# Kernel tuning notes

Hardware: AMD Instinct MI355X
Metric: run time of the kernel (lower is better)

## Reference

```python
import jax, jax.numpy as jnp
import numpy as np

B, S, D, H, NH = 128, 512, 64, 256, 8
HD = H // NH
NEG = -10000000000.0


def _ln(x, g, b, eps=1e-5):
    m = x.mean(-1, keepdims=True)
    v = ((x - m) ** 2).mean(-1, keepdims=True)
    return (x - m) * jax.lax.rsqrt(v + eps) * g + b


def _mha(xq, xkv, mask, qW, qb, kW, kb, vW, vb, oW, ob):
    # mask: [B,1,1,S_kv] bool, True = masked out
    b, sq, _ = xq.shape
    sk = xkv.shape[1]
    Q = (xq @ qW + qb).reshape(b, sq, NH, HD).transpose(0, 2, 1, 3)
    K = (xkv @ kW + kb).reshape(b, sk, NH, HD).transpose(0, 2, 1, 3)
    V = (xkv @ vW + vb).reshape(b, sk, NH, HD).transpose(0, 2, 1, 3)
    energy = jnp.einsum('bhqd,bhkd->bhqk', Q, K) / jnp.sqrt(jnp.float32(HD))
    energy = jnp.where(mask, NEG, energy)
    attn = jax.nn.softmax(energy, axis=-1)  # dropout is identity in eval
    x = jnp.einsum('bhqk,bhkd->bhqd', attn, V)
    x = x.transpose(0, 2, 1, 3).reshape(b, sq, H)
    return x @ oW + ob


def _ffn(x, f1W, f1b, f2W, f2b):
    # NewGELU == tanh-approximate GELU (GPT-2)
    return jax.nn.gelu(x @ f1W + f1b, approximate=True) @ f2W + f2b


def _fwd(src, ln0sg, ln0sb, ln0tg, ln0tb, semW, semb, temW, temb,
         e_qW, e_qb, e_kW, e_kb, e_vW, e_vb, e_oW, e_ob, e_ln1g, e_ln1b,
         e_f1W, e_f1b, e_f2W, e_f2b, e_ln2g, e_ln2b,
         d_sqW, d_sqb, d_skW, d_skb, d_svW, d_svb, d_soW, d_sob, d_ln1g, d_ln1b,
         d_eqW, d_eqb, d_ekW, d_ekb, d_evW, d_evb, d_eoW, d_eob, d_ln2g, d_ln2b,
         d_f1W, d_f1b, d_f2W, d_f2b, d_ln3g, d_ln3b, outW, outb):
    valid = src.sum(-1) != 0                      # [B,S] (prod_fea == 0)
    amask = (~valid)[:, None, None, :]            # [B,1,1,S]; trg==src so trg_mask==src_mask
    embs_src = _ln(src, ln0sg, ln0sb) @ semW + semb   # emb_need
    embs_trg = _ln(src, ln0tg, ln0tb) @ temW + temb
    # encoder layer
    a = _mha(embs_src, embs_src, amask, e_qW, e_qb, e_kW, e_kb, e_vW, e_vb, e_oW, e_ob)
    x = _ln(embs_src + a, e_ln1g, e_ln1b)
    enc_src = _ln(x + _ffn(x, e_f1W, e_f1b, e_f2W, e_f2b), e_ln2g, e_ln2b)
    # decoder layer
    a = _mha(embs_trg, embs_trg, amask, d_sqW, d_sqb, d_skW, d_skb, d_svW, d_svb, d_soW, d_sob)
    t = _ln(embs_trg + a, d_ln1g, d_ln1b)
    a = _mha(t, enc_src, amask, d_eqW, d_eqb, d_ekW, d_ekb, d_evW, d_evb, d_eoW, d_eob)
    t = _ln(t + a, d_ln2g, d_ln2b)
    t = _ln(t + _ffn(t, d_f1W, d_f1b, d_f2W, d_f2b), d_ln3g, d_ln3b)
    logits = (t @ outW + outb)[..., 0]            # [B,S]
    p = jnp.exp(logits) * valid.astype(logits.dtype)
    return p / p.sum(-1, keepdims=True)           # multi_purchase=False branch


def setup_inputs() -> dict:
    key = jax.random.key(0)
    keys = iter(jax.random.split(key, 64))
    inp = {"src": jax.random.normal(next(keys), (B, S, D), dtype=jnp.float32)}

    def lin(name, i, o):
        inp[name + "W"] = jax.random.normal(next(keys), (i, o), dtype=jnp.float32) * 0.02
        inp[name + "b"] = jnp.zeros((o,), dtype=jnp.float32)

    def ln(name, d):
        inp[name + "g"] = jnp.ones((d,), dtype=jnp.float32)
        inp[name + "b"] = jnp.zeros((d,), dtype=jnp.float32)

    ln("ln0s", D); ln("ln0t", D)
    lin("sem", D, H); lin("tem", D, H)
    for n in ["e_q", "e_k", "e_v", "e_o"]:
        lin(n, H, H)
    ln("e_ln1", H); lin("e_f1", H, H); lin("e_f2", H, H); ln("e_ln2", H)
    for n in ["d_sq", "d_sk", "d_sv", "d_so", "d_eq", "d_ek", "d_ev", "d_eo"]:
        lin(n, H, H)
    ln("d_ln1", H); ln("d_ln2", H)
    lin("d_f1", H, H); lin("d_f2", H, H); ln("d_ln3", H)
    lin("out", H, 1)
    return inp


def reference(src, ln0sg, ln0sb, ln0tg, ln0tb, semW, semb, temW, temb,
              e_qW, e_qb, e_kW, e_kb, e_vW, e_vb, e_oW, e_ob, e_ln1g, e_ln1b,
              e_f1W, e_f1b, e_f2W, e_f2b, e_ln2g, e_ln2b,
              d_sqW, d_sqb, d_skW, d_skb, d_svW, d_svb, d_soW, d_sob, d_ln1g, d_ln1b,
              d_eqW, d_eqb, d_ekW, d_ekb, d_evW, d_evb, d_eoW, d_eob, d_ln2g, d_ln2b,
              d_f1W, d_f1b, d_f2W, d_f2b, d_ln3g, d_ln3b, outW, outb):
    return _fwd(src, ln0sg, ln0sb, ln0tg, ln0tb, semW, semb, temW, temb,
                e_qW, e_qb, e_kW, e_kb, e_vW, e_vb, e_oW, e_ob, e_ln1g, e_ln1b,
                e_f1W, e_f1b, e_f2W, e_f2b, e_ln2g, e_ln2b,
                d_sqW, d_sqb, d_skW, d_skb, d_svW, d_svb, d_soW, d_sob, d_ln1g, d_ln1b,
                d_eqW, d_eqb, d_ekW, d_ekb, d_evW, d_evb, d_eoW, d_eob, d_ln2g, d_ln2b,
                d_f1W, d_f1b, d_f2W, d_f2b, d_ln3g, d_ln3b, outW, outb)
```

## Files before the change

kernel.cpp:

```cpp
#include <hip/hip_runtime.h>
#include <hip/hip_bf16.h>


#define Bb  128
#define Ss  512
#define Hh  256
#define NHh 8
#define Mm  (Bb*Ss)

typedef unsigned short bf16_t;
typedef __attribute__((ext_vector_type(8))) short short8;
typedef __attribute__((ext_vector_type(4))) float f32x4;

__device__ __forceinline__ float bf2f(bf16_t h){
  union { unsigned int u; float f; } v; v.u = ((unsigned int)h)<<16; return v.f;
}
__device__ __forceinline__ bf16_t f2bf(float f){
  union { float f; unsigned int u; } v; v.f = f;
  unsigned int r = (v.u + 0x7fffu + ((v.u>>16)&1u)) >> 16;
  return (bf16_t)r;
}
__device__ __forceinline__ unsigned pk_bf16(float a, float b){
  union { __hip_bfloat162 h; unsigned u; } v;
  v.h = __float22bfloat162_rn(float2{a,b});
  return v.u;
}
__device__ __forceinline__ short8 ld_bf8(const bf16_t* p){
  union { uint4 u; short8 s; } v; v.u = *(const uint4*)p; return v.s;
}
__device__ __forceinline__ void gload16(const bf16_t* g, bf16_t* l){
  __builtin_amdgcn_global_load_lds(
      (const __attribute__((address_space(1))) void*)g,
      (__attribute__((address_space(3))) void*)l, 16, 0, 0);
}
__device__ __forceinline__ float exp2_hw(float x){
  float r; asm("v_exp_f32 %0, %1" : "=v"(r) : "v"(x)); return r;
}
__device__ __forceinline__ float gelu_f(float x){
  float u = 0.7978845608028654f*(x + 0.044715f*x*x*x);
  float e = __expf(2.0f*u);
  float th = 1.0f - 2.0f*__builtin_amdgcn_rcpf(e + 1.0f);
  return 0.5f*x*(1.0f + th);
}

struct PrepDesc { const float* s; unsigned off; int K; };
struct Prep18  { PrepDesc d[18]; };

__global__ __launch_bounds__(256) void k_prep(Prep18 p, bf16_t* __restrict__ arena)
{
  PrepDesc dd = p.d[blockIdx.y];
  int i = blockIdx.x*256 + threadIdx.x;
  if (i < dd.K*256){
    int k = i>>8, n = i&255;
    arena[dd.off + n*dd.K + k] = f2bf(dd.s[i]);
  }
}

__global__ __launch_bounds__(256) void k_ln0(const float* __restrict__ src,
    const float* __restrict__ gs, const float* __restrict__ bs,
    const float* __restrict__ gt, const float* __restrict__ bt,
    bf16_t* __restrict__ xs, bf16_t* __restrict__ xt, float* __restrict__ valid)
{
  int row  = blockIdx.x*4 + (threadIdx.x>>6);
  int lane = threadIdx.x & 63;
  float x = src[(size_t)row*64 + lane];
  float s = x;
  #pragma unroll
  for (int o=32;o>0;o>>=1) s += __shfl_xor(s,o);
  float mean = s*(1.0f/64.0f);
  float d = x - mean;
  float ss = d*d;
  #pragma unroll
  for (int o=32;o>0;o>>=1) ss += __shfl_xor(ss,o);
  float r = rsqrtf(ss*(1.0f/64.0f) + 1e-5f);
  float xn = d*r;
  xs[(size_t)row*64+lane] = f2bf(xn*gs[lane] + bs[lane]);
  xt[(size_t)row*64+lane] = f2bf(xn*gt[lane] + bt[lane]);
  if (lane==0) valid[row] = (s != 0.0f) ? 1.0f : 0.0f;
}

template<int EPI, int OUTM, int KK>
__global__ __launch_bounds__(512,2) void k_wgemm(const bf16_t* __restrict__ A,
    const bf16_t* __restrict__ Wt, const float* __restrict__ bias,
    void* __restrict__ Cv, const bf16_t* __restrict__ Pres,
    const float* __restrict__ g, const float* __restrict__ bb,
    const float* __restrict__ oW, const float* __restrict__ obp, float cs)
{
  constexpr int NKC  = KK/32;
  constexpr int IDS  = 16*NKC;
  constexpr int PERW = IDS/8;
  __shared__ bf16_t Ws[IDS*512];

  int t = threadIdx.x, w = t>>6, lane = t&63, l15 = lane&15, quad = lane>>4;
  int r0 = blockIdx.x*256 + w*32;

  #pragma unroll
  for (int j=0; j<PERW; j++){
    int id = w*PERW + j; int kc = id>>4, nt = id&15;
    gload16(Wt + (size_t)(nt*16 + l15)*KK + kc*32 + quad*8, &Ws[id*512]);
  }
  short8 a0 = ld_bf8(A + (size_t)(r0      + l15)*KK + quad*8);
  short8 a1 = ld_bf8(A + (size_t)(r0 + 16 + l15)*KK + quad*8);
  __syncthreads();

  f32x4 z = {0.f,0.f,0.f,0.f};
  f32x4 acc0[16], acc1[16];
  #pragma unroll
  for (int nt=0; nt<16; nt++){ acc0[nt] = z; acc1[nt] = z; }

  #pragma unroll
  for (int kc=0; kc<NKC; kc++){
    short8 a0n, a1n;
    if (kc+1 < NKC){
      a0n = ld_bf8(A + (size_t)(r0      + l15)*KK + (kc+1)*32 + quad*8);
      a1n = ld_bf8(A + (size_t)(r0 + 16 + l15)*KK + (kc+1)*32 + quad*8);
    }
    #pragma unroll
    for (int nt=0; nt<16; nt++){
      short8 b = ld_bf8(&Ws[(kc*16 + nt)*512 + lane*8]);
      acc0[nt] = __builtin_amdgcn_mfma_f32_16x16x32_bf16(a0, b, acc0[nt], 0,0,0);
      acc1[nt] = __builtin_amdgcn_mfma_f32_16x16x32_bf16(a1, b, acc1[nt], 0,0,0);
    }
    a0 = a0n; a1 = a1n;
  }

  float bv[16];
  #pragma unroll
  for (int nt=0; nt<16; nt++) bv[nt] = bias[nt*16 + l15];

  if (OUTM==0){
    auto epi = [&](f32x4 (&ac)[16], int tt){
      int rowb = r0 + tt*16 + quad*4;
      #pragma unroll
      for (int nt=0; nt<16; nt++)
        #pragma unroll
        for (int r=0; r<4; r++){
          float v = ac[nt][r] + bv[nt];
          v = (EPI==1) ? gelu_f(v) : v*cs;
          ((bf16_t*)Cv)[(size_t)(rowb + r)*256 + nt*16 + l15] = f2bf(v);
        }
    };
    epi(acc0, 0); epi(acc1, 1);
  } else if (OUTM==2){
    auto epi = [&](f32x4 (&ac)[16], int tt){
      int m = r0 + tt*16 + quad*4;
      #pragma unroll
      for (int nt=0; nt<16; nt++){
        int col = nt*16 + l15;
        uint2 pk = { pk_bf16(ac[nt][0]+bv[nt], ac[nt][1]+bv[nt]),
                     pk_bf16(ac[nt][2]+bv[nt], ac[nt][3]+bv[nt]) };
        *(uint2*)&((bf16_t*)Cv)[((size_t)((m>>9)*256 + col))*512 + (m&511)] = pk;
      }
    };
    epi(acc0, 0); epi(acc1, 1);
  } else {
    float gv[16], bbv[16], wv[16];
    #pragma unroll
    for (int nt=0; nt<16; nt++){ gv[nt] = g[nt*16+l15]; bbv[nt] = bb[nt*16+l15]; }
    if (OUTM==5)
      #pragma unroll
      for (int nt=0; nt<16; nt++) wv[nt] = oW[nt*16+l15];
    float ob0 = (OUTM==5) ? obp[0] : 0.f;

    auto epi = [&](f32x4 (&ac)[16], int tt){
      #pragma unroll
      for (int r=0; r<4; r++){
        int row = r0 + tt*16 + quad*4 + r;
        const bf16_t* pr = Pres + (size_t)row*256;
        float v[16]; float s = 0.f, q = 0.f;
        #pragma unroll
        for (int nt=0; nt<16; nt++){
          v[nt] = ac[nt][r] + bv[nt] + bf2f(pr[nt*16 + l15]);
          s += v[nt]; q += v[nt]*v[nt];
        }
        s += __shfl_xor(s,1); s += __shfl_xor(s,2);
        s += __shfl_xor(s,4); s += __shfl_xor(s,8);
        q += __shfl_xor(q,1); q += __shfl_xor(q,2);
        q += __shfl_xor(q,4); q += __shfl_xor(q,8);
        float mean = s*(1.0f/256.0f);
        float var  = q*(1.0f/256.0f) - mean*mean;
        float rstd = rsqrtf(var + 1e-5f);
        if (OUTM==3){
          bf16_t* po = (bf16_t*)Cv + (size_t)row*256;
          #pragma unroll
          for (int nt=0; nt<16; nt++)
            po[nt*16 + l15] = f2bf((v[nt]-mean)*rstd*gv[nt] + bbv[nt]);
        } else {
          float s2 = 0.f;
          #pragma unroll
          for (int nt=0; nt<16; nt++)
            s2 += ((v[nt]-mean)*rstd*gv[nt] + bbv[nt]) * wv[nt];
          s2 += __shfl_xor(s2,1); s2 += __shfl_xor(s2,2);
          s2 += __shfl_xor(s2,4); s2 += __shfl_xor(s2,8);
          if (l15==0) ((float*)Cv)[row] = s2 + ob0;
        }
      }
    };
    epi(acc0, 0); epi(acc1, 1);
  }
}

__global__ __launch_bounds__(256) void k_attn(const bf16_t* __restrict__ Qm,
    const bf16_t* __restrict__ Km, const bf16_t* __restrict__ VT,
    const float* __restrict__ valid, bf16_t* __restrict__ AO)
{
  __shared__ bf16_t Pbuf[4][2][2][16][40];
  __shared__ float  Smask[512];
  int t = threadIdx.x, wave = t>>6, lane = t&63, l15 = lane&15, quad = lane>>4;
  int lid = blockIdx.x + 8*blockIdx.y + 1024*blockIdx.z;
  int hp = lid & 3, pb = (lid>>2)&1, g = (lid>>3)&7, bh = lid>>6;
  int h  = hp*2 + (g&1);
  int qc = g>>1;
  int b  = bh*2 + pb;
  int q0 = qc*128;

  Smask[t]     = (valid[b*Ss + t      ] != 0.f) ? 0.f : -1.44269504e10f;
  Smask[t+256] = (valid[b*Ss + t + 256] != 0.f) ? 0.f : -1.44269504e10f;
  __syncthreads();

  short8 aQ0 = ld_bf8(Qm + (size_t)(b*Ss + q0 + (wave*2  )*16 + l15)*256 + h*32 + quad*8);
  short8 aQ1 = ld_bf8(Qm + (size_t)(b*Ss + q0 + (wave*2+1)*16 + l15)*256 + h*32 + quad*8);
  const bf16_t* Kb = Km + (size_t)(b*Ss)*256 + h*32;
  const bf16_t* Vb = VT + ((size_t)b*256 + h*32)*512;

  f32x4 z = {0.f,0.f,0.f,0.f};
  f32x4 O0[2] = {z,z}, O1[2] = {z,z};
  float ls0 = 0.f, ls1 = 0.f;

  auto process = [&](int kt2n, short8 K0, short8 K1){
    int s = kt2n & 1;
    #pragma unroll
    for (int half=0; half<2; half++){
      short8 aK = half ? K1 : K0;
      int ktile = kt2n*2 + half;
      __builtin_amdgcn_s_setprio(1);
      f32x4 s0 = __builtin_amdgcn_mfma_f32_16x16x32_bf16(aK, aQ0, z, 0,0,0);
      f32x4 s1 = __builtin_amdgcn_mfma_f32_16x16x32_bf16(aK, aQ1, z, 0,0,0);
      __builtin_amdgcn_s_setprio(0);
      float4 mb = *(const float4*)&Smask[ktile*16 + quad*4];
      float p00 = exp2_hw(s0[0] + mb.x);
      float p01 = exp2_hw(s0[1] + mb.y);
      float p02 = exp2_hw(s0[2] + mb.z);
      float p03 = exp2_hw(s0[3] + mb.w);
      float p10 = exp2_hw(s1[0] + mb.x);
      float p11 = exp2_hw(s1[1] + mb.y);
      float p12 = exp2_hw(s1[2] + mb.z);
      float p13 = exp2_hw(s1[3] + mb.w);
      ls0 += (p00+p01)+(p02+p03);
      ls1 += (p10+p11)+(p12+p13);
      uint2 w0 = { pk_bf16(p00,p01), pk_bf16(p02,p03) };
      uint2 w1 = { pk_bf16(p10,p11), pk_bf16(p12,p13) };
      *(uint2*)&Pbuf[wave][0][s][l15][half*16 + quad*4] = w0;
      *(uint2*)&Pbuf[wave][1][s][l15][half*16 + quad*4] = w1;
    }
  };
  auto loadK = [&](int n, short8& K0, short8& K1){
    K0 = ld_bf8(Kb + (size_t)((n*2  )*16 + l15)*256 + quad*8);
    K1 = ld_bf8(Kb + (size_t)((n*2+1)*16 + l15)*256 + quad*8);
  };
  auto loadV = [&](int n, short8& V0, short8& V1){
    V0 = ld_bf8(Vb + (size_t)(l15   )*512 + n*32 + quad*8);
    V1 = ld_bf8(Vb + (size_t)(16+l15)*512 + n*32 + quad*8);
  };

  short8 cK0, cK1, pK0, pK1, nK0, nK1;
  short8 cV0, cV1, mV0, mV1, nV0, nV1;
  loadK(0, cK0, cK1);
  process(0, cK0, cK1);
  loadK(1, pK0, pK1);
  loadV(0, cV0, cV1);
  loadV(1, mV0, mV1);

  #pragma unroll 2
  for (int kt2=0; kt2<16; kt2++){
    if (kt2+2 < 16){ loadK(kt2+2, nK0, nK1); loadV(kt2+2, nV0, nV1); }
    int s = kt2 & 1;
    short8 aP0 = ld_bf8(&Pbuf[wave][0][s][l15][quad*8]);
    short8 aP1 = ld_bf8(&Pbuf[wave][1][s][l15][quad*8]);
    __builtin_amdgcn_s_setprio(1);
    O0[0] = __builtin_amdgcn_mfma_f32_16x16x32_bf16(aP0, cV0, O0[0], 0,0,0);
    O0[1] = __builtin_amdgcn_mfma_f32_16x16x32_bf16(aP0, cV1, O0[1], 0,0,0);
    O1[0] = __builtin_amdgcn_mfma_f32_16x16x32_bf16(aP1, cV0, O1[0], 0,0,0);
    O1[1] = __builtin_amdgcn_mfma_f32_16x16x32_bf16(aP1, cV1, O1[1], 0,0,0);
    __builtin_amdgcn_s_setprio(0);
    if (kt2+1 < 16) process(kt2+1, pK0, pK1);
    pK0 = nK0; pK1 = nK1;
    cV0 = mV0; cV1 = mV1; mV0 = nV0; mV1 = nV1;
  }

  ls0 += __shfl_xor(ls0,16); ls0 += __shfl_xor(ls0,32);
  ls1 += __shfl_xor(ls1,16); ls1 += __shfl_xor(ls1,32);
  float linv0 = (ls0 > 0.f) ? 1.0f/ls0 : 0.f;
  float linv1 = (ls1 > 0.f) ? 1.0f/ls1 : 0.f;
  float i0[4], i1[4];
  #pragma unroll
  for (int r=0; r<4; r++){
    i0[r] = __shfl(linv0, quad*4 + r);
    i1[r] = __shfl(linv1, quad*4 + r);
  }
  size_t r0 = (size_t)(b*Ss + q0 + (wave*2  )*16);
  size_t r1 = (size_t)(b*Ss + q0 + (wave*2+1)*16);
  #pragma unroll
  for (int nt=0; nt<2; nt++)
    #pragma unroll
    for (int r=0; r<4; r++){
      AO[(r0 + quad*4 + r)*256 + h*32 + nt*16 + l15] = f2bf(O0[nt][r]*i0[r]);
      AO[(r1 + quad*4 + r)*256 + h*32 + nt*16 + l15] = f2bf(O1[nt][r]*i1[r]);
    }
}

__global__ __launch_bounds__(256) void k_final(const float* __restrict__ L,
    const float* __restrict__ valid, float* __restrict__ out)
{
  __shared__ float wsum[4];
  int b = blockIdx.x, t = threadIdx.x;
  float e0 = __expf(L[b*Ss + t      ]) * valid[b*Ss + t      ];
  float e1 = __expf(L[b*Ss + 256 + t]) * valid[b*Ss + 256 + t];
  float s = e0 + e1;
  #pragma unroll
  for (int o=32;o>0;o>>=1) s += __shfl_xor(s,o);
  if ((t&63)==0) wsum[t>>6] = s;
  __syncthreads();
  float tot = wsum[0]+wsum[1]+wsum[2]+wsum[3];
  out[b*Ss + t      ] = e0/tot;
  out[b*Ss + 256 + t] = e1/tot;
}

extern "C" void kernel_launch(void* const* d_in, const int* in_sizes, int n_in,
                              void* d_out, int out_size, void* d_ws, size_t ws_size,
                              hipStream_t stream)
{
  #define F(i) ((const float*)d_in[(i)])
  bool sig = (in_sizes[33] == 256);
  const float* d_eqW  = F(sig?35:33); const float* d_eqb  = F(sig?36:34);
  const float* d_ekW  = F(sig?37:35); const float* d_ekb  = F(sig?38:36);
  const float* d_evW  = F(sig?39:37); const float* d_evb  = F(sig?40:38);
  const float* d_eoW  = F(sig?41:39); const float* d_eob  = F(sig?42:40);
  const float* d_ln1g = F(sig?33:41); const float* d_ln1b = F(sig?34:42);

  char* w = (char*)d_ws;
  bf16_t* P0 = (bf16_t*)w; w += (size_t)Mm*Hh*2;
  bf16_t* P1 = (bf16_t*)w; w += (size_t)Mm*Hh*2;
  bf16_t* H0 = (bf16_t*)w; w += (size_t)Mm*Hh*2;
  bf16_t* H1 = (bf16_t*)w;
  bf16_t* xs = (bf16_t*)w; w += (size_t)Mm*Hh*2;
  bf16_t* H2 = (bf16_t*)w;
  bf16_t* xt = (bf16_t*)w; w += (size_t)Mm*Hh*2;
  bf16_t* Wa = (bf16_t*)w; w += (size_t)(2*16384 + 16*65536)*2;
  float*  valid  = (float*)w; w += (size_t)Mm*4;
  float*  logits = (float*)w; w += (size_t)Mm*4;
  float* out = (float*)d_out;

  unsigned o_sem = 0, o_tem = 16384;
  unsigned o_w[16]; for (int i=0;i<16;i++) o_w[i] = 32768 + i*65536u;
  Prep18 pp;
  const float* srcs[18] = { F(5), F(7), F(9), F(11), F(13), F(15), F(19), F(21),
                            F(25), F(27), F(29), F(31), d_eqW, d_ekW, d_evW, d_eoW,
                            F(45), F(47) };
  unsigned offs[18] = { o_sem, o_tem, o_w[0],o_w[1],o_w[2],o_w[3],o_w[4],o_w[5],
                        o_w[6],o_w[7],o_w[8],o_w[9],o_w[10],o_w[11],o_w[12],o_w[13],
                        o_w[14],o_w[15] };
  for (int i=0;i<18;i++){ pp.d[i].s = srcs[i]; pp.d[i].off = offs[i]; pp.d[i].K = (i<2)?64:256; }

  dim3 blk(256);
  dim3 blk512(512);
  dim3 gLN(Mm/4);
  dim3 gW(256);
  dim3 gA(NHh, Bb, 4);
  dim3 gP(256, 18);
  const float* NF = nullptr; const bf16_t* NB = nullptr;
  const float QS = 0.17677669529663687f * 1.4426950408889634f;

  k_prep<<<gP, blk, 0, stream>>>(pp, Wa);
  k_ln0<<<gLN, blk, 0, stream>>>(F(0), F(1),F(2), F(3),F(4), xs, xt, valid);

  k_wgemm<0,0,64><<<gW, blk512, 0, stream>>>(xs, Wa+o_sem, F(6), P0, NB, NF,NF,NF,NF, 1.0f);
  k_wgemm<0,0,64><<<gW, blk512, 0, stream>>>(xt, Wa+o_tem, F(8), P1, NB, NF,NF,NF,NF, 1.0f);

  k_wgemm<0,0,256><<<gW, blk512, 0, stream>>>(P0, Wa+o_w[0], F(10), H0, NB, NF,NF,NF,NF, QS);
  k_wgemm<0,0,256><<<gW, blk512, 0, stream>>>(P0, Wa+o_w[1], F(12), H1, NB, NF,NF,NF,NF, 1.0f);
  k_wgemm<0,2,256><<<gW, blk512, 0, stream>>>(P0, Wa+o_w[2], F(14), H2, NB, NF,NF,NF,NF, 1.0f);
  k_attn<<<gA, blk, 0, stream>>>(H0, H1, H2, valid, H0);
  k_wgemm<0,3,256><<<gW, blk512, 0, stream>>>(H0, Wa+o_w[3], F(16), P0, P0, F(17),F(18), NF,NF, 1.0f);
  k_wgemm<1,0,256><<<gW, blk512, 0, stream>>>(P0, Wa+o_w[4], F(20), H0, NB, NF,NF,NF,NF, 1.0f);
  k_wgemm<0,3,256><<<gW, blk512, 0, stream>>>(H0, Wa+o_w[5], F(22), P0, P0, F(23),F(24), NF,NF, 1.0f);

  k_wgemm<0,0,256><<<gW, blk512, 0, stream>>>(P1, Wa+o_w[6], F(26), H0, NB, NF,NF,NF,NF, QS);
  k_wgemm<0,0,256><<<gW, blk512, 0, stream>>>(P1, Wa+o_w[7], F(28), H1, NB, NF,NF,NF,NF, 1.0f);
  k_wgemm<0,2,256><<<gW, blk512, 0, stream>>>(P1, Wa+o_w[8], F(30), H2, NB, NF,NF,NF,NF, 1.0f);
  k_attn<<<gA, blk, 0, stream>>>(H0, H1, H2, valid, H0);
  k_wgemm<0,3,256><<<gW, blk512, 0, stream>>>(H0, Wa+o_w[9], F(32), P1, P1, d_ln1g,d_ln1b, NF,NF, 1.0f);

  k_wgemm<0,0,256><<<gW, blk512, 0, stream>>>(P1, Wa+o_w[10], d_eqb, H0, NB, NF,NF,NF,NF, QS);
  k_wgemm<0,0,256><<<gW, blk512, 0, stream>>>(P0, Wa+o_w[11], d_ekb, H1, NB, NF,NF,NF,NF, 1.0f);
  k_wgemm<0,2,256><<<gW, blk512, 0, stream>>>(P0, Wa+o_w[12], d_evb, H2, NB, NF,NF,NF,NF, 1.0f);
  k_attn<<<gA, blk, 0, stream>>>(H0, H1, H2, valid, H0);
  k_wgemm<0,3,256><<<gW, blk512, 0, stream>>>(H0, Wa+o_w[13], d_eob, P1, P1, F(43),F(44), NF,NF, 1.0f);

  k_wgemm<1,0,256><<<gW, blk512, 0, stream>>>(P1, Wa+o_w[14], F(46), H0, NB, NF,NF,NF,NF, 1.0f);
  k_wgemm<0,5,256><<<gW, blk512, 0, stream>>>(H0, Wa+o_w[15], F(48), logits, P1, F(49),F(50), F(51),F(52), 1.0f);

  k_final<<<dim3(Bb), blk, 0, stream>>>(logits, valid, out);
  #undef F
}
```

Baseline: 929.2 us.

## Split non-LayerNorm GEMMs into column halves and deepen attention K prefetch

The weight GEMM kernel gains an output-width template parameter. GEMMs without a row-wise LayerNorm epilogue now run with 512 blocks, each computing 128 output columns, instead of 256 blocks covering all 256 columns. This is meant to improve occupancy and load balance across CUs and to halve the LDS weight footprint and accumulator registers per block, at the cost of each block reloading its A rows. In the attention kernel, K tiles are prefetched three steps ahead and the softmax/QK processing of the next tile is issued before the PV MFMAs rather than after, to overlap memory latency better, which adds register pressure.

```diff
diff --git a/kernel.cpp b/kernel.cpp
--- a/kernel.cpp
+++ b/kernel.cpp
@@ -79,7 +79,7 @@
   if (lane==0) valid[row] = (s != 0.0f) ? 1.0f : 0.0f;
 }
 
-template<int EPI, int OUTM, int KK>
+template<int EPI, int OUTM, int KK, int NN>
 __global__ __launch_bounds__(512,2) void k_wgemm(const bf16_t* __restrict__ A,
     const bf16_t* __restrict__ Wt, const float* __restrict__ bias,
     void* __restrict__ Cv, const bf16_t* __restrict__ Pres,
@@ -87,26 +87,29 @@
     const float* __restrict__ oW, const float* __restrict__ obp, float cs)
 {
   constexpr int NKC  = KK/32;
-  constexpr int IDS  = 16*NKC;
+  constexpr int NT16 = NN/16;
+  constexpr int IDS  = NT16*NKC;
   constexpr int PERW = IDS/8;
   __shared__ bf16_t Ws[IDS*512];
 
   int t = threadIdx.x, w = t>>6, lane = t&63, l15 = lane&15, quad = lane>>4;
-  int r0 = blockIdx.x*256 + w*32;
+  int rowblk = (NN==256) ? blockIdx.x : (blockIdx.x>>1);
+  int c0     = (NN==256) ? 0 : (blockIdx.x&1)*NN;
+  int r0 = rowblk*256 + w*32;
 
   #pragma unroll
   for (int j=0; j<PERW; j++){
-    int id = w*PERW + j; int kc = id>>4, nt = id&15;
-    gload16(Wt + (size_t)(nt*16 + l15)*KK + kc*32 + quad*8, &Ws[id*512]);
+    int id = w*PERW + j; int kc = id/NT16, nt = id%NT16;
+    gload16(Wt + (size_t)(c0 + nt*16 + l15)*KK + kc*32 + quad*8, &Ws[id*512]);
   }
   short8 a0 = ld_bf8(A + (size_t)(r0      + l15)*KK + quad*8);
   short8 a1 = ld_bf8(A + (size_t)(r0 + 16 + l15)*KK + quad*8);
   __syncthreads();
 
   f32x4 z = {0.f,0.f,0.f,0.f};
-  f32x4 acc0[16], acc1[16];
-  #pragma unroll
-  for (int nt=0; nt<16; nt++){ acc0[nt] = z; acc1[nt] = z; }
+  f32x4 acc0[NT16], acc1[NT16];
+  #pragma unroll
+  for (int nt=0; nt<NT16; nt++){ acc0[nt] = z; acc1[nt] = z; }
 
   #pragma unroll
   for (int kc=0; kc<NKC; kc++){
@@ -116,37 +119,37 @@
       a1n = ld_bf8(A + (size_t)(r0 + 16 + l15)*KK + (kc+1)*32 + quad*8);
     }
     #pragma unroll
-    for (int nt=0; nt<16; nt++){
-      short8 b = ld_bf8(&Ws[(kc*16 + nt)*512 + lane*8]);
+    for (int nt=0; nt<NT16; nt++){
+      short8 b = ld_bf8(&Ws[(kc*NT16 + nt)*512 + lane*8]);
       acc0[nt] = __builtin_amdgcn_mfma_f32_16x16x32_bf16(a0, b, acc0[nt], 0,0,0);
       acc1[nt] = __builtin_amdgcn_mfma_f32_16x16x32_bf16(a1, b, acc1[nt], 0,0,0);
     }
     a0 = a0n; a1 = a1n;
   }
 
-  float bv[16];
-  #pragma unroll
-  for (int nt=0; nt<16; nt++) bv[nt] = bias[nt*16 + l15];
+  float bv[NT16];
+  #pragma unroll
+  for (int nt=0; nt<NT16; nt++) bv[nt] = bias[c0 + nt*16 + l15];
 
   if (OUTM==0){
-    auto epi = [&](f32x4 (&ac)[16], int tt){
+    auto epi = [&](f32x4 (&ac)[NT16], int tt){
       int rowb = r0 + tt*16 + quad*4;
       #pragma unroll
-      for (int nt=0; nt<16; nt++)
+      for (int nt=0; nt<NT16; nt++)
         #pragma unroll
         for (int r=0; r<4; r++){
           float v = ac[nt][r] + bv[nt];
           v = (EPI==1) ? gelu_f(v) : v*cs;
-          ((bf16_t*)Cv)[(size_t)(rowb + r)*256 + nt*16 + l15] = f2bf(v);
+          ((bf16_t*)Cv)[(size_t)(rowb + r)*256 + c0 + nt*16 + l15] = f2bf(v);
         }
     };
     epi(acc0, 0); epi(acc1, 1);
   } else if (OUTM==2){
-    auto epi = [&](f32x4 (&ac)[16], int tt){
+    auto epi = [&](f32x4 (&ac)[NT16], int tt){
       int m = r0 + tt*16 + quad*4;
       #pragma unroll
-      for (int nt=0; nt<16; nt++){
-        int col = nt*16 + l15;
+      for (int nt=0; nt<NT16; nt++){
+        int col = c0 + nt*16 + l15;
         uint2 pk = { pk_bf16(ac[nt][0]+bv[nt], ac[nt][1]+bv[nt]),
                      pk_bf16(ac[nt][2]+bv[nt], ac[nt][3]+bv[nt]) };
         *(uint2*)&((bf16_t*)Cv)[((size_t)((m>>9)*256 + col))*512 + (m&511)] = pk;
@@ -154,22 +157,22 @@
     };
     epi(acc0, 0); epi(acc1, 1);
   } else {
-    float gv[16], bbv[16], wv[16];
+    float gv[NT16], bbv[NT16], wv[NT16];
     #pragma unroll
-    for (int nt=0; nt<16; nt++){ gv[nt] = g[nt*16+l15]; bbv[nt] = bb[nt*16+l15]; }
+    for (int nt=0; nt<NT16; nt++){ gv[nt] = g[nt*16+l15]; bbv[nt] = bb[nt*16+l15]; }
     if (OUTM==5)
       #pragma unroll
-      for (int nt=0; nt<16; nt++) wv[nt] = oW[nt*16+l15];
+      for (int nt=0; nt<NT16; nt++) wv[nt] = oW[nt*16+l15];
     float ob0 = (OUTM==5) ? obp[0] : 0.f;
 
-    auto epi = [&](f32x4 (&ac)[16], int tt){
+    auto epi = [&](f32x4 (&ac)[NT16], int tt){
       #pragma unroll
       for (int r=0; r<4; r++){
         int row = r0 + tt*16 + quad*4 + r;
         const bf16_t* pr = Pres + (size_t)row*256;
-        float v[16]; float s = 0.f, q = 0.f;
+        float v[NT16]; float s = 0.f, q = 0.f;
         #pragma unroll
-        for (int nt=0; nt<16; nt++){
+        for (int nt=0; nt<NT16; nt++){
           v[nt] = ac[nt][r] + bv[nt] + bf2f(pr[nt*16 + l15]);
           s += v[nt]; q += v[nt]*v[nt];
         }
@@ -183,12 +186,12 @@
         if (OUTM==3){
           bf16_t* po = (bf16_t*)Cv + (size_t)row*256;
           #pragma unroll
-          for (int nt=0; nt<16; nt++)
+          for (int nt=0; nt<NT16; nt++)
             po[nt*16 + l15] = f2bf((v[nt]-mean)*rstd*gv[nt] + bbv[nt]);
         } else {
           float s2 = 0.f;
           #pragma unroll
-          for (int nt=0; nt<16; nt++)
+          for (int nt=0; nt<NT16; nt++)
             s2 += ((v[nt]-mean)*rstd*gv[nt] + bbv[nt]) * wv[nt];
           s2 += __shfl_xor(s2,1); s2 += __shfl_xor(s2,2);
           s2 += __shfl_xor(s2,4); s2 += __shfl_xor(s2,8);
@@ -263,17 +266,20 @@
     V1 = ld_bf8(Vb + (size_t)(16+l15)*512 + n*32 + quad*8);
   };
 
-  short8 cK0, cK1, pK0, pK1, nK0, nK1;
+  short8 cK0, cK1, pK0, pK1, nK0, nK1, qK0, qK1;
   short8 cV0, cV1, mV0, mV1, nV0, nV1;
   loadK(0, cK0, cK1);
-  process(0, cK0, cK1);
   loadK(1, pK0, pK1);
+  loadK(2, nK0, nK1);
   loadV(0, cV0, cV1);
   loadV(1, mV0, mV1);
+  process(0, cK0, cK1);
 
   #pragma unroll 2
   for (int kt2=0; kt2<16; kt2++){
-    if (kt2+2 < 16){ loadK(kt2+2, nK0, nK1); loadV(kt2+2, nV0, nV1); }
+    if (kt2+3 < 16) loadK(kt2+3, qK0, qK1);
+    if (kt2+2 < 16) loadV(kt2+2, nV0, nV1);
+    if (kt2+1 < 16) process(kt2+1, pK0, pK1);
     int s = kt2 & 1;
     short8 aP0 = ld_bf8(&Pbuf[wave][0][s][l15][quad*8]);
     short8 aP1 = ld_bf8(&Pbuf[wave][1][s][l15][quad*8]);
@@ -283,8 +289,7 @@
     O1[0] = __builtin_amdgcn_mfma_f32_16x16x32_bf16(aP1, cV0, O1[0], 0,0,0);
     O1[1] = __builtin_amdgcn_mfma_f32_16x16x32_bf16(aP1, cV1, O1[1], 0,0,0);
     __builtin_amdgcn_s_setprio(0);
-    if (kt2+1 < 16) process(kt2+1, pK0, pK1);
-    pK0 = nK0; pK1 = nK1;
+    pK0 = nK0; pK1 = nK1; nK0 = qK0; nK1 = qK1;
     cV0 = mV0; cV1 = mV1; mV0 = nV0; mV1 = nV1;
   }
 
@@ -366,6 +371,7 @@
   dim3 blk512(512);
   dim3 gLN(Mm/4);
   dim3 gW(256);
+  dim3 gW2(512);
   dim3 gA(NHh, Bb, 4);
   dim3 gP(256, 18);
   const float* NF = nullptr; const bf16_t* NB = nullptr;
@@ -374,31 +380,31 @@
   k_prep<<<gP, blk, 0, stream>>>(pp, Wa);
   k_ln0<<<gLN, blk, 0, stream>>>(F(0), F(1),F(2), F(3),F(4), xs, xt, valid);
 
-  k_wgemm<0,0,64><<<gW, blk512, 0, stream>>>(xs, Wa+o_sem, F(6), P0, NB, NF,NF,NF,NF, 1.0f);
-  k_wgemm<0,0,64><<<gW, blk512, 0, stream>>>(xt, Wa+o_tem, F(8), P1, NB, NF,NF,NF,NF, 1.0f);
-
-  k_wgemm<0,0,256><<<gW, blk512, 0, stream>>>(P0, Wa+o_w[0], F(10), H0, NB, NF,NF,NF,NF, QS);
-  k_wgemm<0,0,256><<<gW, blk512, 0, stream>>>(P0, Wa+o_w[1], F(12), H1, NB, NF,NF,NF,NF, 1.0f);
-  k_wgemm<0,2,256><<<gW, blk512, 0, stream>>>(P0, Wa+o_w[2], F(14), H2, NB, NF,NF,NF,NF, 1.0f);
+  k_wgemm<0,0,64,128><<<gW2, blk512, 0, stream>>>(xs, Wa+o_sem, F(6), P0, NB, NF,NF,NF,NF, 1.0f);
+  k_wgemm<0,0,64,128><<<gW2, blk512, 0, stream>>>(xt, Wa+o_tem, F(8), P1, NB, NF,NF,NF,NF, 1.0f);
+
+  k_wgemm<0,0,256,128><<<gW2, blk512, 0, stream>>>(P0, Wa+o_w[0], F(10), H0, NB, NF,NF,NF,NF, QS);
+  k_wgemm<0,0,256,128><<<gW2, blk512, 0, stream>>>(P0, Wa+o_w[1], F(12), H1, NB, NF,NF,NF,NF, 1.0f);
+  k_wgemm<0,2,256,128><<<gW2, blk512, 0, stream>>>(P0, Wa+o_w[2], F(14), H2, NB, NF,NF,NF,NF, 1.0f);
   k_attn<<<gA, blk, 0, stream>>>(H0, H1, H2, valid, H0);
-  k_wgemm<0,3,256><<<gW, blk512, 0, stream>>>(H0, Wa+o_w[3], F(16), P0, P0, F(17),F(18), NF,NF, 1.0f);
-  k_wgemm<1,0,256><<<gW, blk512, 0, stream>>>(P0, Wa+o_w[4], F(20), H0, NB, NF,NF,NF,NF, 1.0f);
-  k_wgemm<0,3,256><<<gW, blk512, 0, stream>>>(H0, Wa+o_w[5], F(22), P0, P0, F(23),F(24), NF,NF, 1.0f);
-
-  k_wgemm<0,0,256><<<gW, blk512, 0, stream>>>(P1, Wa+o_w[6], F(26), H0, NB, NF,NF,NF,NF, QS);
-  k_wgemm<0,0,256><<<gW, blk512, 0, stream>>>(P1, Wa+o_w[7], F(28), H1, NB, NF,NF,NF,NF, 1.0f);
-  k_wgemm<0,2,256><<<gW, blk512, 0, stream>>>(P1, Wa+o_w[8], F(30), H2, NB, NF,NF,NF,NF, 1.0f);
+  k_wgemm<0,3,256,256><<<gW, blk512, 0, stream>>>(H0, Wa+o_w[3], F(16), P0, P0, F(17),F(18), NF,NF, 1.0f);
+  k_wgemm<1,0,256,128><<<gW2, blk512, 0, stream>>>(P0, Wa+o_w[4], F(20), H0, NB, NF,NF,NF,NF, 1.0f);
+  k_wgemm<0,3,256,256><<<gW, blk512, 0, stream>>>(H0, Wa+o_w[5], F(22), P0, P0, F(23),F(24), NF,NF, 1.0f);
+
+  k_wgemm<0,0,256,128><<<gW2, blk512, 0, stream>>>(P1, Wa+o_w[6], F(26), H0, NB, NF,NF,NF,NF, QS);
+  k_wgemm<0,0,256,128><<<gW2, blk512, 0, stream>>>(P1, Wa+o_w[7], F(28), H1, NB, NF,NF,NF,NF, 1.0f);
+  k_wgemm<0,2,256,128><<<gW2, blk512, 0, stream>>>(P1, Wa+o_w[8], F(30), H2, NB, NF,NF,NF,NF, 1.0f);
   k_attn<<<gA, blk, 0, stream>>>(H0, H1, H2, valid, H0);
-  k_wgemm<0,3,256><<<gW, blk512, 0, stream>>>(H0, Wa+o_w[9], F(32), P1, P1, d_ln1g,d_ln1b, NF,NF, 1.0f);
-
-  k_wgemm<0,0,256><<<gW, blk512, 0, stream>>>(P1, Wa+o_w[10], d_eqb, H0, NB, NF,NF,NF,NF, QS);
-  k_wgemm<0,0,256><<<gW, blk512, 0, stream>>>(P0, Wa+o_w[11], d_ekb, H1, NB, NF,NF,NF,NF, 1.0f);
-  k_wgemm<0,2,256><<<gW, blk512, 0, stream>>>(P0, Wa+o_w[12], d_evb, H2, NB, NF,NF,NF,NF, 1.0f);
+  k_wgemm<0,3,256,256><<<gW, blk512, 0, stream>>>(H0, Wa+o_w[9], F(32), P1, P1, d_ln1g,d_ln1b, NF,NF, 1.0f);
+
+  k_wgemm<0,0,256,128><<<gW2, blk512, 0, stream>>>(P1, Wa+o_w[10], d_eqb, H0, NB, NF,NF,NF,NF, QS);
+  k_wgemm<0,0,256,128><<<gW2, blk512, 0, stream>>>(P0, Wa+o_w[11], d_ekb, H1, NB, NF,NF,NF,NF, 1.0f);
+  k_wgemm<0,2,256,128><<<gW2, blk512, 0, stream>>>(P0, Wa+o_w[12], d_evb, H2, NB, NF,NF,NF,NF, 1.0f);
   k_attn<<<gA, blk, 0, stream>>>(H0, H1, H2, valid, H0);
-  k_wgemm<0,3,256><<<gW, blk512, 0, stream>>>(H0, Wa+o_w[13], d_eob, P1, P1, F(43),F(44), NF,NF, 1.0f);
-
-  k_wgemm<1,0,256><<<gW, blk512, 0, stream>>>(P1, Wa+o_w[14], F(46), H0, NB, NF,NF,NF,NF, 1.0f);
-  k_wgemm<0,5,256><<<gW, blk512, 0, stream>>>(H0, Wa+o_w[15], F(48), logits, P1, F(49),F(50), F(51),F(52), 1.0f);
+  k_wgemm<0,3,256,256><<<gW, blk512, 0, stream>>>(H0, Wa+o_w[13], d_eob, P1, P1, F(43),F(44), NF,NF, 1.0f);
+
+  k_wgemm<1,0,256,128><<<gW2, blk512, 0, stream>>>(P1, Wa+o_w[14], F(46), H0, NB, NF,NF,NF,NF, 1.0f);
+  k_wgemm<0,5,256,256><<<gW, blk512, 0, stream>>>(H0, Wa+o_w[15], F(48), logits, P1, F(49),F(50), F(51),F(52), 1.0f);
 
   k_final<<<dim3(Bb), blk, 0, stream>>>(logits, valid, out);
   #undef F
```

After: 948.7 us. +2.1%, slower.

## Batch QKV projections into one launch and pipeline weight staging and attention loads

Applied to the files above, without the earlier changes.

Groups the Q/K/V projection GEMMs, and the two embedding GEMMs, into single launches that use blockIdx.y to pick a job, so the GPU fills with more blocks per launch and pays fewer launch gaps. The shared GEMM core now stages only half the weight tile up front. The second half is held in registers and written to LDS after the first half of the K loop, and A fragments are prefetched two steps ahead. The attention loop prefetches K one tile further and issues the softmax step before the PV MFMAs to overlap better. This raises register pressure and adds an extra barrier per GEMM.

```diff
diff --git a/kernel.cpp b/kernel.cpp
--- a/kernel.cpp
+++ b/kernel.cpp
@@ -79,50 +79,137 @@
   if (lane==0) valid[row] = (s != 0.0f) ? 1.0f : 0.0f;
 }
 
+template<int KK>
+__device__ __forceinline__ void wgemm_core(const bf16_t* __restrict__ A,
+    const bf16_t* __restrict__ Wt, bf16_t* Ws,
+    int r0, int w, int lane, int l15, int quad,
+    f32x4 (&acc0)[16], f32x4 (&acc1)[16])
+{
+  constexpr int NKC = KK/32;
+  constexpr int H1  = NKC/2;
+  constexpr int WH  = NKC;
+
+  short8 af[3][2];
+  af[0][0] = ld_bf8(A + (size_t)(r0      + l15)*KK + quad*8);
+  af[0][1] = ld_bf8(A + (size_t)(r0 + 16 + l15)*KK + quad*8);
+  af[1][0] = ld_bf8(A + (size_t)(r0      + l15)*KK + 32 + quad*8);
+  af[1][1] = ld_bf8(A + (size_t)(r0 + 16 + l15)*KK + 32 + quad*8);
+
+  #pragma unroll
+  for (int j=0; j<H1*2; j++){
+    int kc = j>>1, nt = w*2 + (j&1);
+    gload16(Wt + (size_t)(nt*16 + l15)*KK + kc*32 + quad*8,
+            &Ws[(kc*16 + nt)*512]);
+  }
+  __syncthreads();
+
+  uint4 wreg[H1*2];
+  #pragma unroll
+  for (int j=0; j<H1*2; j++){
+    int kc = H1 + (j>>1), nt = w*2 + (j&1);
+    wreg[j] = *(const uint4*)(Wt + (size_t)(nt*16 + l15)*KK + kc*32 + quad*8);
+  }
+
+  f32x4 z = {0.f,0.f,0.f,0.f};
+  #pragma unroll
+  for (int nt=0; nt<16; nt++){ acc0[nt] = z; acc1[nt] = z; }
+
+  #pragma unroll
+  for (int kc=0; kc<H1; kc++){
+    if (kc+2 < NKC){
+      af[(kc+2)%3][0] = ld_bf8(A + (size_t)(r0      + l15)*KK + (kc+2)*32 + quad*8);
+      af[(kc+2)%3][1] = ld_bf8(A + (size_t)(r0 + 16 + l15)*KK + (kc+2)*32 + quad*8);
+    }
+    short8 a0 = af[kc%3][0], a1 = af[kc%3][1];
+    #pragma unroll
+    for (int nt=0; nt<16; nt++){
+      short8 b = ld_bf8(&Ws[(kc*16 + nt)*512 + lane*8]);
+      acc0[nt] = __builtin_amdgcn_mfma_f32_16x16x32_bf16(a0, b, acc0[nt], 0,0,0);
+      acc1[nt] = __builtin_amdgcn_mfma_f32_16x16x32_bf16(a1, b, acc1[nt], 0,0,0);
+    }
+  }
+  #pragma unroll
+  for (int j=0; j<H1*2; j++){
+    int kc = H1 + (j>>1), nt = w*2 + (j&1);
+    *(uint4*)&Ws[(kc*16 + nt)*512 + lane*8] = wreg[j];
+  }
+  __syncthreads();
+  #pragma unroll
+  for (int kc=H1; kc<NKC; kc++){
+    if (kc+2 < NKC){
+      af[(kc+2)%3][0] = ld_bf8(A + (size_t)(r0      + l15)*KK + (kc+2)*32 + quad*8);
+      af[(kc+2)%3][1] = ld_bf8(A + (size_t)(r0 + 16 + l15)*KK + (kc+2)*32 + quad*8);
+    }
+    short8 a0 = af[kc%3][0], a1 = af[kc%3][1];
+    #pragma unroll
+    for (int nt=0; nt<16; nt++){
+      short8 b = ld_bf8(&Ws[(kc*16 + nt)*512 + lane*8]);
+      acc0[nt] = __builtin_amdgcn_mfma_f32_16x16x32_bf16(a0, b, acc0[nt], 0,0,0);
+      acc1[nt] = __builtin_amdgcn_mfma_f32_16x16x32_bf16(a1, b, acc1[nt], 0,0,0);
+    }
+  }
+}
+
+struct WJob  { const bf16_t* A; const bf16_t* Wt; const float* bias; bf16_t* C;
+               int outm; float cs; };
+struct WJobs { WJob j[3]; };
+
+template<int KK>
+__global__ __launch_bounds__(512,2) void k_wqkv(WJobs jobs)
+{
+  constexpr int NKC = KK/32;
+  __shared__ bf16_t Ws[16*NKC*512];
+  WJob jb = jobs.j[blockIdx.y];
+  int t = threadIdx.x, w = t>>6, lane = t&63, l15 = lane&15, quad = lane>>4;
+  int r0 = blockIdx.x*256 + w*32;
+
+  f32x4 acc0[16], acc1[16];
+  wgemm_core<KK>(jb.A, jb.Wt, Ws, r0, w, lane, l15, quad, acc0, acc1);
+
+  float bv[16];
+  #pragma unroll
+  for (int nt=0; nt<16; nt++) bv[nt] = jb.bias[nt*16 + l15];
+
+  if (jb.outm == 0){
+    float cs = jb.cs;
+    auto epi = [&](f32x4 (&ac)[16], int tt){
+      int rowb = r0 + tt*16 + quad*4;
+      #pragma unroll
+      for (int nt=0; nt<16; nt++)
+        #pragma unroll
+        for (int r=0; r<4; r++)
+          jb.C[(size_t)(rowb + r)*256 + nt*16 + l15] = f2bf((ac[nt][r] + bv[nt])*cs);
+    };
+    epi(acc0, 0); epi(acc1, 1);
+  } else {
+    auto epi = [&](f32x4 (&ac)[16], int tt){
+      int m = r0 + tt*16 + quad*4;
+      #pragma unroll
+      for (int nt=0; nt<16; nt++){
+        int col = nt*16 + l15;
+        uint2 pk = { pk_bf16(ac[nt][0]+bv[nt], ac[nt][1]+bv[nt]),
+                     pk_bf16(ac[nt][2]+bv[nt], ac[nt][3]+bv[nt]) };
+        *(uint2*)&jb.C[((size_t)((m>>9)*256 + col))*512 + (m&511)] = pk;
+      }
+    };
+    epi(acc0, 0); epi(acc1, 1);
+  }
+}
+
 template<int EPI, int OUTM, int KK>
 __global__ __launch_bounds__(512,2) void k_wgemm(const bf16_t* __restrict__ A,
     const bf16_t* __restrict__ Wt, const float* __restrict__ bias,
     void* __restrict__ Cv, const bf16_t* __restrict__ Pres,
     const float* __restrict__ g, const float* __restrict__ bb,
-    const float* __restrict__ oW, const float* __restrict__ obp, float cs)
-{
-  constexpr int NKC  = KK/32;
-  constexpr int IDS  = 16*NKC;
-  constexpr int PERW = IDS/8;
-  __shared__ bf16_t Ws[IDS*512];
-
+    const float* __restrict__ oW, const float* __restrict__ obp)
+{
+  constexpr int NKC = KK/32;
+  __shared__ bf16_t Ws[16*NKC*512];
   int t = threadIdx.x, w = t>>6, lane = t&63, l15 = lane&15, quad = lane>>4;
   int r0 = blockIdx.x*256 + w*32;
 
-  #pragma unroll
-  for (int j=0; j<PERW; j++){
-    int id = w*PERW + j; int kc = id>>4, nt = id&15;
-    gload16(Wt + (size_t)(nt*16 + l15)*KK + kc*32 + quad*8, &Ws[id*512]);
-  }
-  short8 a0 = ld_bf8(A + (size_t)(r0      + l15)*KK + quad*8);
-  short8 a1 = ld_bf8(A + (size_t)(r0 + 16 + l15)*KK + quad*8);
-  __syncthreads();
-
-  f32x4 z = {0.f,0.f,0.f,0.f};
   f32x4 acc0[16], acc1[16];
-  #pragma unroll
-  for (int nt=0; nt<16; nt++){ acc0[nt] = z; acc1[nt] = z; }
-
-  #pragma unroll
-  for (int kc=0; kc<NKC; kc++){
-    short8 a0n, a1n;
-    if (kc+1 < NKC){
-      a0n = ld_bf8(A + (size_t)(r0      + l15)*KK + (kc+1)*32 + quad*8);
-      a1n = ld_bf8(A + (size_t)(r0 + 16 + l15)*KK + (kc+1)*32 + quad*8);
-    }
-    #pragma unroll
-    for (int nt=0; nt<16; nt++){
-      short8 b = ld_bf8(&Ws[(kc*16 + nt)*512 + lane*8]);
-      acc0[nt] = __builtin_amdgcn_mfma_f32_16x16x32_bf16(a0, b, acc0[nt], 0,0,0);
-      acc1[nt] = __builtin_amdgcn_mfma_f32_16x16x32_bf16(a1, b, acc1[nt], 0,0,0);
-    }
-    a0 = a0n; a1 = a1n;
-  }
+  wgemm_core<KK>(A, Wt, Ws, r0, w, lane, l15, quad, acc0, acc1);
 
   float bv[16];
   #pragma unroll
@@ -136,21 +223,9 @@
         #pragma unroll
         for (int r=0; r<4; r++){
           float v = ac[nt][r] + bv[nt];
-          v = (EPI==1) ? gelu_f(v) : v*cs;
+          if (EPI==1) v = gelu_f(v);
           ((bf16_t*)Cv)[(size_t)(rowb + r)*256 + nt*16 + l15] = f2bf(v);
         }
-    };
-    epi(acc0, 0); epi(acc1, 1);
-  } else if (OUTM==2){
-    auto epi = [&](f32x4 (&ac)[16], int tt){
-      int m = r0 + tt*16 + quad*4;
-      #pragma unroll
-      for (int nt=0; nt<16; nt++){
-        int col = nt*16 + l15;
-        uint2 pk = { pk_bf16(ac[nt][0]+bv[nt], ac[nt][1]+bv[nt]),
-                     pk_bf16(ac[nt][2]+bv[nt], ac[nt][3]+bv[nt]) };
-        *(uint2*)&((bf16_t*)Cv)[((size_t)((m>>9)*256 + col))*512 + (m&511)] = pk;
-      }
     };
     epi(acc0, 0); epi(acc1, 1);
   } else {
@@ -263,17 +338,20 @@
     V1 = ld_bf8(Vb + (size_t)(16+l15)*512 + n*32 + quad*8);
   };
 
-  short8 cK0, cK1, pK0, pK1, nK0, nK1;
+  short8 cK0, cK1, pK0, pK1, nK0, nK1, qK0, qK1;
   short8 cV0, cV1, mV0, mV1, nV0, nV1;
   loadK(0, cK0, cK1);
-  process(0, cK0, cK1);
   loadK(1, pK0, pK1);
+  loadK(2, nK0, nK1);
   loadV(0, cV0, cV1);
   loadV(1, mV0, mV1);
+  process(0, cK0, cK1);
 
   #pragma unroll 2
   for (int kt2=0; kt2<16; kt2++){
-    if (kt2+2 < 16){ loadK(kt2+2, nK0, nK1); loadV(kt2+2, nV0, nV1); }
+    if (kt2+3 < 16) loadK(kt2+3, qK0, qK1);
+    if (kt2+2 < 16) loadV(kt2+2, nV0, nV1);
+    if (kt2+1 < 16) process(kt2+1, pK0, pK1);
     int s = kt2 & 1;
     short8 aP0 = ld_bf8(&Pbuf[wave][0][s][l15][quad*8]);
     short8 aP1 = ld_bf8(&Pbuf[wave][1][s][l15][quad*8]);
@@ -283,8 +361,7 @@
     O1[0] = __builtin_amdgcn_mfma_f32_16x16x32_bf16(aP1, cV0, O1[0], 0,0,0);
     O1[1] = __builtin_amdgcn_mfma_f32_16x16x32_bf16(aP1, cV1, O1[1], 0,0,0);
     __builtin_amdgcn_s_setprio(0);
-    if (kt2+1 < 16) process(kt2+1, pK0, pK1);
-    pK0 = nK0; pK1 = nK1;
+    pK0 = nK0; pK1 = nK1; nK0 = qK0; nK1 = qK1;
     cV0 = mV0; cV1 = mV1; mV0 = nV0; mV1 = nV1;
   }
 
@@ -374,31 +451,48 @@
   k_prep<<<gP, blk, 0, stream>>>(pp, Wa);
   k_ln0<<<gLN, blk, 0, stream>>>(F(0), F(1),F(2), F(3),F(4), xs, xt, valid);
 
-  k_wgemm<0,0,64><<<gW, blk512, 0, stream>>>(xs, Wa+o_sem, F(6), P0, NB, NF,NF,NF,NF, 1.0f);
-  k_wgemm<0,0,64><<<gW, blk512, 0, stream>>>(xt, Wa+o_tem, F(8), P1, NB, NF,NF,NF,NF, 1.0f);
-
-  k_wgemm<0,0,256><<<gW, blk512, 0, stream>>>(P0, Wa+o_w[0], F(10), H0, NB, NF,NF,NF,NF, QS);
-  k_wgemm<0,0,256><<<gW, blk512, 0, stream>>>(P0, Wa+o_w[1], F(12), H1, NB, NF,NF,NF,NF, 1.0f);
-  k_wgemm<0,2,256><<<gW, blk512, 0, stream>>>(P0, Wa+o_w[2], F(14), H2, NB, NF,NF,NF,NF, 1.0f);
+  {
+    WJobs js;
+    js.j[0] = { xs, Wa+o_sem, F(6), P0, 0, 1.0f };
+    js.j[1] = { xt, Wa+o_tem, F(8), P1, 0, 1.0f };
+    js.j[2] = js.j[0];
+    k_wqkv<64><<<dim3(256,2), blk512, 0, stream>>>(js);
+  }
+
+  {
+    WJobs js;
+    js.j[0] = { P0, Wa+o_w[0], F(10), H0, 0, QS  };
+    js.j[1] = { P0, Wa+o_w[1], F(12), H1, 0, 1.0f };
+    js.j[2] = { P0, Wa+o_w[2], F(14), H2, 2, 1.0f };
+    k_wqkv<256><<<dim3(256,3), blk512, 0, stream>>>(js);
+  }
   k_attn<<<gA, blk, 0, stream>>>(H0, H1, H2, valid, H0);
-  k_wgemm<0,3,256><<<gW, blk512, 0, stream>>>(H0, Wa+o_w[3], F(16), P0, P0, F(17),F(18), NF,NF, 1.0f);
-  k_wgemm<1,0,256><<<gW, blk512, 0, stream>>>(P0, Wa+o_w[4], F(20), H0, NB, NF,NF,NF,NF, 1.0f);
-  k_wgemm<0,3,256><<<gW, blk512, 0, stream>>>(H0, Wa+o_w[5], F(22), P0, P0, F(23),F(24), NF,NF, 1.0f);
-
-  k_wgemm<0,0,256><<<gW, blk512, 0, stream>>>(P1, Wa+o_w[6], F(26), H0, NB, NF,NF,NF,NF, QS);
-  k_wgemm<0,0,256><<<gW, blk512, 0, stream>>>(P1, Wa+o_w[7], F(28), H1, NB, NF,NF,NF,NF, 1.0f);
-  k_wgemm<0,2,256><<<gW, blk512, 0, stream>>>(P1, Wa+o_w[8], F(30), H2, NB, NF,NF,NF,NF, 1.0f);
+  k_wgemm<0,3,256><<<gW, blk512, 0, stream>>>(H0, Wa+o_w[3], F(16), P0, P0, F(17),F(18), NF,NF);
+  k_wgemm<1,0,256><<<gW, blk512, 0, stream>>>(P0, Wa+o_w[4], F(20), H0, NB, NF,NF,NF,NF);
+  k_wgemm<0,3,256><<<gW, blk512, 0, stream>>>(H0, Wa+o_w[5], F(22), P0, P0, F(23),F(24), NF,NF);
+
+  {
+    WJobs js;
+    js.j[0] = { P1, Wa+o_w[6], F(26), H0, 0, QS  };
+    js.j[1] = { P1, Wa+o_w[7], F(28), H1, 0, 1.0f };
+    js.j[2] = { P1, Wa+o_w[8], F(30), H2, 2, 1.0f };
+    k_wqkv<256><<<dim3(256,3), blk512, 0, stream>>>(js);
+  }
   k_attn<<<gA, blk, 0, stream>>>(H0, H1, H2, valid, H0);
-  k_wgemm<0,3,256><<<gW, blk512, 0, stream>>>(H0, Wa+o_w[9], F(32), P1, P1, d_ln1g,d_ln1b, NF,NF, 1.0f);
-
-  k_wgemm<0,0,256><<<gW, blk512, 0, stream>>>(P1, Wa+o_w[10], d_eqb, H0, NB, NF,NF,NF,NF, QS);
-  k_wgemm<0,0,256><<<gW, blk512, 0, stream>>>(P0, Wa+o_w[11], d_ekb, H1, NB, NF,NF,NF,NF, 1.0f);
-  k_wgemm<0,2,256><<<gW, blk512, 0, stream>>>(P0, Wa+o_w[12], d_evb, H2, NB, NF,NF,NF,NF, 1.0f);
+  k_wgemm<0,3,256><<<gW, blk512, 0, stream>>>(H0, Wa+o_w[9], F(32), P1, P1, d_ln1g,d_ln1b, NF,NF);
+
+  {
+    WJobs js;
+    js.j[0] = { P1, Wa+o_w[10], d_eqb, H0, 0, QS  };
+    js.j[1] = { P0, Wa+o_w[11], d_ekb, H1, 0, 1.0f };
+    js.j[2] = { P0, Wa+o_w[12], d_evb, H2, 2, 1.0f };
+    k_wqkv<256><<<dim3(256,3), blk512, 0, stream>>>(js);
+  }
   k_attn<<<gA, blk, 0, stream>>>(H0, H1, H2, valid, H0);
-  k_wgemm<0,3,256><<<gW, blk512, 0, stream>>>(H0, Wa+o_w[13], d_eob, P1, P1, F(43),F(44), NF,NF, 1.0f);
-
-  k_wgemm<1,0,256><<<gW, blk512, 0, stream>>>(P1, Wa+o_w[14], F(46), H0, NB, NF,NF,NF,NF, 1.0f);
-  k_wgemm<0,5,256><<<gW, blk512, 0, stream>>>(H0, Wa+o_w[15], F(48), logits, P1, F(49),F(50), F(51),F(52), 1.0f);
+  k_wgemm<0,3,256><<<gW, blk512, 0, stream>>>(H0, Wa+o_w[13], d_eob, P1, P1, F(43),F(44), NF,NF);
+
+  k_wgemm<1,0,256><<<gW, blk512, 0, stream>>>(P1, Wa+o_w[14], F(46), H0, NB, NF,NF,NF,NF);
+  k_wgemm<0,5,256><<<gW, blk512, 0, stream>>>(H0, Wa+o_w[15], F(48), logits, P1, F(49),F(50), F(51),F(52));
 
   k_final<<<dim3(Bb), blk, 0, stream>>>(logits, valid, out);
   #undef F
```

Result: slower. 1.317 ms (+41.7%).
